# Kernel optimization log

Hardware: AMD Instinct MI355X
Metric: run time of the kernel (lower is better)

## Reference

```python
import jax, jax.numpy as jnp
import numpy as np

BZ, SEQ, IN_SZ, HID_SZ = 256, 512, 256, 256


def setup_inputs() -> dict:
    key = jax.random.key(0)
    k1, k2, k3, k4, k5 = jax.random.split(key, 5)
    stdv = 1.0 / np.sqrt(HID_SZ)
    return {
        "encoder_inputs": jax.random.normal(k1, (BZ, HID_SZ), dtype=jnp.float32),
        "decoder_inputs": jax.random.normal(k2, (BZ, SEQ, IN_SZ), dtype=jnp.float32),
        "U_i": jax.random.uniform(k3, (IN_SZ, HID_SZ), minval=-stdv, maxval=stdv, dtype=jnp.float32),
        "V_i": jax.random.uniform(k4, (HID_SZ, HID_SZ), minval=-stdv, maxval=stdv, dtype=jnp.float32),
        "b_i": jax.random.uniform(k5, (HID_SZ,), minval=-stdv, maxval=stdv, dtype=jnp.float32),
    }


def reference(encoder_inputs, decoder_inputs, U_i, V_i, b_i):
    # Sequential vanilla-RNN recurrence over time via lax.scan.
    # h_t = tanh(x_t @ U_i + h_{t-1} @ V_i + b_i)
    xs = jnp.swapaxes(decoder_inputs, 0, 1)  # [seq, bz, in]

    def step(h, x_t):
        h_new = jnp.tanh(x_t @ U_i + h @ V_i + b_i)
        return h_new, h_new

    _, outs = jax.lax.scan(step, encoder_inputs, xs)  # outs: [seq, bz, hid]
    decoder_outputs = jnp.swapaxes(outs, 0, 1)  # [bz, seq, hid]
    return (encoder_inputs, decoder_outputs)
```

## Files before the change

kernel.cpp:

```cpp
#include <hip/hip_runtime.h>
#include <hip/hip_bf16.h>


#define SEQn 512
#define HIDn 256

typedef __attribute__((ext_vector_type(4))) float  floatx4;
typedef __attribute__((ext_vector_type(8))) short  short8;

__device__ __forceinline__ short f2bf(float f) {
    __hip_bfloat16 h = __float2bfloat16(f);
    return *reinterpret_cast<short*>(&h);
}

__global__ void prep_B(const float* __restrict__ U, short* __restrict__ wsB) {
    int idx = blockIdx.x * 256 + threadIdx.x;
    int n  = idx & 255;
    int q  = (idx >> 8) & 3;
    int kb = idx >> 10;
    int k0 = kb * 32 + q * 8;
    short8 c;
    #pragma unroll
    for (int j = 0; j < 8; j++)
        c[j] = f2bf(U[(size_t)(k0 + j) * 256 + n]);
    *(short8*)(wsB + (size_t)idx * 8) = c;
}

__global__ __launch_bounds__(256, 4)
void xu_gemm(const float* __restrict__ X, const short* __restrict__ wsB,
             const float* __restrict__ bias, float* __restrict__ out)
{
    const int tid = threadIdx.x;
    const int l   = tid & 63;
    const int w   = tid >> 6;
    const int lr  = l & 15;
    const int q   = l >> 4;
    const int m0  = blockIdx.y * 128;
    const int n0  = blockIdx.x * 128;

    floatx4 acc[2][8];
    #pragma unroll
    for (int mt = 0; mt < 2; mt++)
        #pragma unroll
        for (int nt = 0; nt < 8; nt++)
            acc[mt][nt] = (floatx4){0.f, 0.f, 0.f, 0.f};

    const size_t rowA = (size_t)(m0 + 32 * w + lr);

    for (int kb = 0; kb < 8; kb++) {
        short8 af[2];
        #pragma unroll
        for (int mt = 0; mt < 2; mt++) {
            const float* p = X + (rowA + 16 * mt) * 256 + kb * 32 + q * 8;
            float4 a0 = *(const float4*)p;
            float4 a1 = *(const float4*)(p + 4);
            af[mt][0] = f2bf(a0.x); af[mt][1] = f2bf(a0.y);
            af[mt][2] = f2bf(a0.z); af[mt][3] = f2bf(a0.w);
            af[mt][4] = f2bf(a1.x); af[mt][5] = f2bf(a1.y);
            af[mt][6] = f2bf(a1.z); af[mt][7] = f2bf(a1.w);
        }
        #pragma unroll
        for (int nt = 0; nt < 8; nt++) {
            short8 bfr = *(const short8*)(wsB +
                ((size_t)(kb * 4 + q) * 256 + n0 + 16 * nt + lr) * 8);
            acc[0][nt] = __builtin_amdgcn_mfma_f32_16x16x32_bf16(af[0], bfr, acc[0][nt], 0, 0, 0);
            acc[1][nt] = __builtin_amdgcn_mfma_f32_16x16x32_bf16(af[1], bfr, acc[1][nt], 0, 0, 0);
        }
    }

    #pragma unroll
    for (int nt = 0; nt < 8; nt++) {
        float bv = bias[n0 + 16 * nt + lr];
        #pragma unroll
        for (int mt = 0; mt < 2; mt++) {
            #pragma unroll
            for (int r = 0; r < 4; r++) {
                int row = m0 + 32 * w + 16 * mt + 4 * q + r;
                out[(size_t)row * 256 + n0 + 16 * nt + lr] = acc[mt][nt][r] + bv;
            }
        }
    }
}

__global__ __launch_bounds__(512, 2)
void rnn_rec(const float* __restrict__ enc, const float* __restrict__ V,
             float* __restrict__ out)
{
    __shared__ float hbuf[HIDn];
    __shared__ float part[8][HIDn];

    const int tid = threadIdx.x;
    const int w   = tid >> 6;
    const int l   = tid & 63;
    const int b   = blockIdx.x;

    float4 v[32];
    #pragma unroll
    for (int kk = 0; kk < 32; kk++)
        v[kk] = *(const float4*)(V + (size_t)(32 * w + kk) * 256 + 4 * l);

    float* outEnc = out + (size_t)b * HIDn;
    float* outDec = out + (size_t)65536 + (size_t)b * SEQn * HIDn;

    if (tid < HIDn) {
        float h0 = enc[(size_t)b * HIDn + tid];
        hbuf[tid]   = h0;
        outEnc[tid] = h0;
    }
    float xu_cur = 0.f;
    if (tid < HIDn) xu_cur = outDec[tid];
    __syncthreads();

    for (int t = 0; t < SEQn; t++) {
        float xu_next = 0.f;
        if (tid < HIDn && t + 1 < SEQn)
            xu_next = outDec[(size_t)(t + 1) * HIDn + tid];

        float hv = hbuf[32 * w + (l & 31)];
        int   hvi = __builtin_bit_cast(int, hv);

        float4 acc = make_float4(0.f, 0.f, 0.f, 0.f);
        #pragma unroll
        for (int kk = 0; kk < 32; kk++) {
            float hs = __builtin_bit_cast(float, __builtin_amdgcn_readlane(hvi, kk));
            float4 vv = v[kk];
            acc.x = fmaf(hs, vv.x, acc.x);
            acc.y = fmaf(hs, vv.y, acc.y);
            acc.z = fmaf(hs, vv.z, acc.z);
            acc.w = fmaf(hs, vv.w, acc.w);
        }
        *(float4*)&part[w][4 * l] = acc;
        __syncthreads();

        if (tid < HIDn) {
            float s = xu_cur;
            #pragma unroll
            for (int ww = 0; ww < 8; ww++) s += part[ww][tid];
            float e = __expf(2.f * s);
            float h = 1.f - 2.f / (e + 1.f);
            hbuf[tid] = h;
            outDec[(size_t)t * HIDn + tid] = h;
        }
        xu_cur = xu_next;
        __syncthreads();
    }
}

extern "C" void kernel_launch(void* const* d_in, const int* in_sizes, int n_in,
                              void* d_out, int out_size, void* d_ws, size_t ws_size,
                              hipStream_t stream) {
    const float* enc  = (const float*)d_in[0];
    const float* x    = (const float*)d_in[1];
    const float* U    = (const float*)d_in[2];
    const float* V    = (const float*)d_in[3];
    const float* bias = (const float*)d_in[4];
    float* out = (float*)d_out;

    float* outDec = out + 65536;

    short* wsB = (ws_size >= 131072) ? (short*)d_ws : (short*)out;

    prep_B<<<32, 256, 0, stream>>>(U, wsB);

    dim3 ggrid(2, 1024);
    xu_gemm<<<ggrid, 256, 0, stream>>>(x, wsB, bias, outDec);

    rnn_rec<<<256, 512, 0, stream>>>(enc, V, out);
}
```

Before: 604.6 us.

## Fuse input projection into recurrence kernel using bf16 MFMA for both matmuls

Removes the separate X·U GEMM kernel and computes both x_t·U and h·V inside the per-batch recurrence loop with bf16 MFMA. The weights are kept in registers as MFMA fragments, and the hidden state and input row are double-buffered in LDS as bf16. This halves the barriers per step and removes the large intermediate write and re-read of the projected inputs. In exchange each step does more MFMA work on a single-row (mostly idle) tile, and the hidden state is rounded to bf16 on every step, which can let error accumulate over the 512-step recurrence.

```diff
diff --git a/kernel.cpp b/kernel.cpp
--- a/kernel.cpp
+++ b/kernel.cpp
@@ -7,142 +7,122 @@
 
 typedef __attribute__((ext_vector_type(4))) float  floatx4;
 typedef __attribute__((ext_vector_type(8))) short  short8;
+typedef __attribute__((ext_vector_type(4))) short  shortx4;
 
 __device__ __forceinline__ short f2bf(float f) {
     __hip_bfloat16 h = __float2bfloat16(f);
     return *reinterpret_cast<short*>(&h);
 }
 
-__global__ void prep_B(const float* __restrict__ U, short* __restrict__ wsB) {
+__global__ void prep_W(const float* __restrict__ U, const float* __restrict__ V,
+                       short* __restrict__ wsU, short* __restrict__ wsV) {
     int idx = blockIdx.x * 256 + threadIdx.x;
-    int n  = idx & 255;
-    int q  = (idx >> 8) & 3;
-    int kb = idx >> 10;
-    int k0 = kb * 32 + q * 8;
-    short8 c;
+    int col = idx & 255;
+    int q   = (idx >> 8) & 3;
+    int kb  = idx >> 10;
+    int k0  = kb * 32 + q * 8;
+    short8 cu, cv;
     #pragma unroll
-    for (int j = 0; j < 8; j++)
-        c[j] = f2bf(U[(size_t)(k0 + j) * 256 + n]);
-    *(short8*)(wsB + (size_t)idx * 8) = c;
-}
-
-__global__ __launch_bounds__(256, 4)
-void xu_gemm(const float* __restrict__ X, const short* __restrict__ wsB,
-             const float* __restrict__ bias, float* __restrict__ out)
-{
-    const int tid = threadIdx.x;
-    const int l   = tid & 63;
-    const int w   = tid >> 6;
-    const int lr  = l & 15;
-    const int q   = l >> 4;
-    const int m0  = blockIdx.y * 128;
-    const int n0  = blockIdx.x * 128;
-
-    floatx4 acc[2][8];
-    #pragma unroll
-    for (int mt = 0; mt < 2; mt++)
-        #pragma unroll
-        for (int nt = 0; nt < 8; nt++)
-            acc[mt][nt] = (floatx4){0.f, 0.f, 0.f, 0.f};
-
-    const size_t rowA = (size_t)(m0 + 32 * w + lr);
-
-    for (int kb = 0; kb < 8; kb++) {
-        short8 af[2];
-        #pragma unroll
-        for (int mt = 0; mt < 2; mt++) {
-            const float* p = X + (rowA + 16 * mt) * 256 + kb * 32 + q * 8;
-            float4 a0 = *(const float4*)p;
-            float4 a1 = *(const float4*)(p + 4);
-            af[mt][0] = f2bf(a0.x); af[mt][1] = f2bf(a0.y);
-            af[mt][2] = f2bf(a0.z); af[mt][3] = f2bf(a0.w);
-            af[mt][4] = f2bf(a1.x); af[mt][5] = f2bf(a1.y);
-            af[mt][6] = f2bf(a1.z); af[mt][7] = f2bf(a1.w);
-        }
-        #pragma unroll
-        for (int nt = 0; nt < 8; nt++) {
-            short8 bfr = *(const short8*)(wsB +
-                ((size_t)(kb * 4 + q) * 256 + n0 + 16 * nt + lr) * 8);
-            acc[0][nt] = __builtin_amdgcn_mfma_f32_16x16x32_bf16(af[0], bfr, acc[0][nt], 0, 0, 0);
-            acc[1][nt] = __builtin_amdgcn_mfma_f32_16x16x32_bf16(af[1], bfr, acc[1][nt], 0, 0, 0);
-        }
+    for (int j = 0; j < 8; j++) {
+        cu[j] = f2bf(U[(size_t)(k0 + j) * 256 + col]);
+        cv[j] = f2bf(V[(size_t)(k0 + j) * 256 + col]);
     }
-
-    #pragma unroll
-    for (int nt = 0; nt < 8; nt++) {
-        float bv = bias[n0 + 16 * nt + lr];
-        #pragma unroll
-        for (int mt = 0; mt < 2; mt++) {
-            #pragma unroll
-            for (int r = 0; r < 4; r++) {
-                int row = m0 + 32 * w + 16 * mt + 4 * q + r;
-                out[(size_t)row * 256 + n0 + 16 * nt + lr] = acc[mt][nt][r] + bv;
-            }
-        }
-    }
+    *(short8*)(wsU + (size_t)idx * 8) = cu;
+    *(short8*)(wsV + (size_t)idx * 8) = cv;
 }
 
 __global__ __launch_bounds__(512, 2)
-void rnn_rec(const float* __restrict__ enc, const float* __restrict__ V,
-             float* __restrict__ out)
+void rnn_fused(const float* __restrict__ enc, const float* __restrict__ x,
+               const float* __restrict__ bias,
+               const short* __restrict__ wsU, const short* __restrict__ wsV,
+               float* __restrict__ out)
 {
-    __shared__ float hbuf[HIDn];
-    __shared__ float part[8][HIDn];
+    __shared__ short hb[2][HIDn];
+    __shared__ short xb[2][HIDn];
 
     const int tid = threadIdx.x;
     const int w   = tid >> 6;
     const int l   = tid & 63;
+    const int lr  = l & 15;
+    const int q   = l >> 4;
     const int b   = blockIdx.x;
 
-    float4 v[32];
+    short8 uf[8][2], vf[8][2];
     #pragma unroll
-    for (int kk = 0; kk < 32; kk++)
-        v[kk] = *(const float4*)(V + (size_t)(32 * w + kk) * 256 + 4 * l);
+    for (int kb = 0; kb < 8; kb++)
+        #pragma unroll
+        for (int nt = 0; nt < 2; nt++) {
+            size_t base = ((size_t)(kb * 4 + q) * 256 + 32 * w + 16 * nt + lr) * 8;
+            uf[kb][nt] = *(const short8*)(wsU + base);
+            vf[kb][nt] = *(const short8*)(wsV + base);
+        }
 
-    float* outEnc = out + (size_t)b * HIDn;
-    float* outDec = out + (size_t)65536 + (size_t)b * SEQn * HIDn;
+    const float* xrow   = x + (size_t)b * SEQn * HIDn;
+    float*       outDec = out + (size_t)65536 + (size_t)b * SEQn * HIDn;
 
-    if (tid < HIDn) {
-        float h0 = enc[(size_t)b * HIDn + tid];
-        hbuf[tid]   = h0;
-        outEnc[tid] = h0;
+    const float bias0 = bias[32 * w + lr];
+    const float bias1 = bias[32 * w + 16 + lr];
+
+    float4 xr_next = make_float4(0.f, 0.f, 0.f, 0.f);
+    if (l < 8) {
+        int c0 = 32 * w + 4 * l;
+        float4 h4 = *(const float4*)(enc + (size_t)b * HIDn + c0);
+        *(shortx4*)&hb[0][c0] = (shortx4){f2bf(h4.x), f2bf(h4.y), f2bf(h4.z), f2bf(h4.w)};
+        float4 x0 = *(const float4*)(xrow + c0);
+        *(shortx4*)&xb[0][c0] = (shortx4){f2bf(x0.x), f2bf(x0.y), f2bf(x0.z), f2bf(x0.w)};
+        xr_next = *(const float4*)(xrow + HIDn + c0);
     }
-    float xu_cur = 0.f;
-    if (tid < HIDn) xu_cur = outDec[tid];
     __syncthreads();
 
     for (int t = 0; t < SEQn; t++) {
-        float xu_next = 0.f;
-        if (tid < HIDn && t + 1 < SEQn)
-            xu_next = outDec[(size_t)(t + 1) * HIDn + tid];
+        const int cur = t & 1, nxt = cur ^ 1;
 
-        float hv = hbuf[32 * w + (l & 31)];
-        int   hvi = __builtin_bit_cast(int, hv);
+        float4 xr2 = xr_next;
+        if (l < 8) {
+            int t2 = (t + 2 < SEQn) ? t + 2 : SEQn - 1;
+            xr2 = *(const float4*)(xrow + (size_t)t2 * HIDn + 32 * w + 4 * l);
+        }
 
-        float4 acc = make_float4(0.f, 0.f, 0.f, 0.f);
+        floatx4 acc0 = (floatx4){0.f, 0.f, 0.f, 0.f};
+        floatx4 acc1 = (floatx4){0.f, 0.f, 0.f, 0.f};
+        const short* xp = &xb[cur][q * 8];
+        const short* hp = &hb[cur][q * 8];
         #pragma unroll
-        for (int kk = 0; kk < 32; kk++) {
-            float hs = __builtin_bit_cast(float, __builtin_amdgcn_readlane(hvi, kk));
-            float4 vv = v[kk];
-            acc.x = fmaf(hs, vv.x, acc.x);
-            acc.y = fmaf(hs, vv.y, acc.y);
-            acc.z = fmaf(hs, vv.z, acc.z);
-            acc.w = fmaf(hs, vv.w, acc.w);
+        for (int kb = 0; kb < 8; kb++) {
+            short8 xa = *(const short8*)(xp + kb * 32);
+            short8 ha = *(const short8*)(hp + kb * 32);
+            acc0 = __builtin_amdgcn_mfma_f32_16x16x32_bf16(xa, uf[kb][0], acc0, 0, 0, 0);
+            acc1 = __builtin_amdgcn_mfma_f32_16x16x32_bf16(xa, uf[kb][1], acc1, 0, 0, 0);
+            acc0 = __builtin_amdgcn_mfma_f32_16x16x32_bf16(ha, vf[kb][0], acc0, 0, 0, 0);
+            acc1 = __builtin_amdgcn_mfma_f32_16x16x32_bf16(ha, vf[kb][1], acc1, 0, 0, 0);
         }
-        *(float4*)&part[w][4 * l] = acc;
+
+        if (l < 8) {
+            int c0 = 32 * w + 4 * l;
+            *(shortx4*)&xb[nxt][c0] =
+                (shortx4){f2bf(xr_next.x), f2bf(xr_next.y), f2bf(xr_next.z), f2bf(xr_next.w)};
+        }
+
+        if (q == 0) {
+            float s0 = acc0[0] + bias0;
+            float s1 = acc1[0] + bias1;
+            float e0 = __expf(2.f * s0);
+            float e1 = __expf(2.f * s1);
+            float h0 = 1.f - 2.f / (e0 + 1.f);
+            float h1 = 1.f - 2.f / (e1 + 1.f);
+            int c = 32 * w + lr;
+            hb[nxt][c]      = f2bf(h0);
+            hb[nxt][c + 16] = f2bf(h1);
+            outDec[(size_t)t * HIDn + c]      = h0;
+            outDec[(size_t)t * HIDn + c + 16] = h1;
+        }
+        xr_next = xr2;
         __syncthreads();
+    }
 
-        if (tid < HIDn) {
-            float s = xu_cur;
-            #pragma unroll
-            for (int ww = 0; ww < 8; ww++) s += part[ww][tid];
-            float e = __expf(2.f * s);
-            float h = 1.f - 2.f / (e + 1.f);
-            hbuf[tid] = h;
-            outDec[(size_t)t * HIDn + tid] = h;
-        }
-        xu_cur = xu_next;
-        __syncthreads();
+    if (tid < 64) {
+        float4 e = *(const float4*)(enc + (size_t)b * HIDn + 4 * tid);
+        *(float4*)(out + (size_t)b * HIDn + 4 * tid) = e;
     }
 }
 
@@ -156,14 +136,15 @@
     const float* bias = (const float*)d_in[4];
     float* out = (float*)d_out;
 
-    float* outDec = out + 65536;
+    short *wsU, *wsV;
+    if (ws_size >= 262144) {
+        wsU = (short*)d_ws;
+        wsV = wsU + 65536;
+    } else {
+        wsU = (short*)out;
+        wsV = wsU + 65536;
+    }
 
-    short* wsB = (ws_size >= 131072) ? (short*)d_ws : (short*)out;
-
-    prep_B<<<32, 256, 0, stream>>>(U, wsB);
-
-    dim3 ggrid(2, 1024);
-    xu_gemm<<<ggrid, 256, 0, stream>>>(x, wsB, bias, outDec);
-
-    rnn_rec<<<256, 512, 0, stream>>>(enc, V, out);
+    prep_W<<<32, 256, 0, stream>>>(U, V, wsU, wsV);
+    rnn_fused<<<256, 512, 0, stream>>>(enc, x, bias, wsU, wsV, out);
 }
```

Result: slower. 639.6 us (+5.8%).
